# Performance work log

Measured on AMD Instinct MI355X. Metric: run time of the kernel, lower is better.

## Reference

```python
import jax, jax.numpy as jnp
import numpy as np

N = 8192          # points per cloud
IN_C = 256        # in_channels
OUT_C = 256       # out_channels
SC = IN_C // 4    # shortcut_out_channels
KNN = 32          # neighbors gathered per point
KP = 15           # kernel points (standard KPConv)
RADIUS = 0.12
EXTENT = RADIUS * 2.0 / 2.5   # radius * kp_extent / conv_radius
NEG_SLOPE = 0.1
EPS = 1e-5


def setup_inputs() -> dict:
    key = jax.random.key(0)
    ks = jax.random.split(key, 10)
    src = jax.random.normal(ks[0], (N, IN_C), jnp.float32)
    tgt = jax.random.normal(ks[1], (N, IN_C), jnp.float32)
    src_coords = jax.random.uniform(ks[2], (N, 3), jnp.float32)
    tgt_coords = jax.random.uniform(ks[3], (N, 3), jnp.float32)
    W_in = jax.random.normal(ks[4], (IN_C, SC), jnp.float32) / np.sqrt(IN_C)
    b_in = jnp.zeros((SC,), jnp.float32)
    kernel_pts = jax.random.normal(ks[5], (KP, 3), jnp.float32) * (0.7 * EXTENT)
    W_kp = jax.random.normal(ks[6], (KP, SC, SC), jnp.float32) / np.sqrt(KP * SC)
    W_out = jax.random.normal(ks[7], (SC, OUT_C), jnp.float32) / np.sqrt(SC)
    b_out = jnp.zeros((OUT_C,), jnp.float32)
    gamma = jnp.ones((OUT_C,), jnp.float32)
    beta = jnp.zeros((OUT_C,), jnp.float32)
    return dict(src=src, tgt=tgt, src_coords=src_coords, tgt_coords=tgt_coords,
                W_in=W_in, b_in=b_in, kernel_pts=kernel_pts, W_kp=W_kp,
                W_out=W_out, b_out=b_out, gamma=gamma, beta=beta)


def _one_cloud(x, coords, W_in, b_in, kernel_pts, W_kp, W_out, b_out, gamma, beta):
    # 1x1 conv in: [N, IN_C] -> [N, SC]
    h = x @ W_in + b_in

    # neighbor search: kNN by squared distance, masked to the conv radius
    d2 = jnp.sum((coords[:, None, :] - coords[None, :, :]) ** 2, axis=-1)  # [N, N]
    _, idx = jax.lax.top_k(-d2, KNN)                                       # [N, KNN]
    nb_coords = coords[idx]                                                # [N, KNN, 3]
    rel = nb_coords - coords[:, None, :]                                   # [N, KNN, 3]
    in_range = jnp.sum(rel ** 2, axis=-1) <= RADIUS ** 2                   # [N, KNN]

    # KPConv: linear correlation to kernel points, masked neighbor aggregate
    diff = rel[:, :, None, :] - kernel_pts[None, None, :, :]               # [N, KNN, KP, 3]
    dist = jnp.sqrt(jnp.sum(diff ** 2, axis=-1))                           # [N, KNN, KP]
    infl = jnp.maximum(1.0 - dist / EXTENT, 0.0) * in_range[:, :, None]    # [N, KNN, KP]
    nb_feats = h[idx]                                                      # [N, KNN, SC]
    agg = jnp.einsum('nkp,nkc->npc', infl, nb_feats)                       # [N, KP, SC]
    h = jnp.einsum('npc,pcd->nd', agg, W_kp)                               # [N, SC]

    # 1x1 conv out: [N, SC] -> [N, OUT_C]
    y = h @ W_out + b_out

    # batch norm over points (training-mode statistics) + affine
    mu = jnp.mean(y, axis=0)
    var = jnp.mean((y - mu) ** 2, axis=0)
    y = gamma * (y - mu) * jax.lax.rsqrt(var + EPS) + beta

    # leaky relu
    return jnp.where(y > 0, y, NEG_SLOPE * y)


def reference(src, tgt, src_coords, tgt_coords, W_in, b_in, kernel_pts, W_kp,
              W_out, b_out, gamma, beta):
    params = (W_in, b_in, kernel_pts, W_kp, W_out, b_out, gamma, beta)
    s = _one_cloud(src, src_coords, *params)
    t = _one_cloud(tgt, tgt_coords, *params)
    return (s, t, src_coords, tgt_coords)
```

## Files before the change

kernel.cpp:

```cpp
#include <hip/hip_runtime.h>
#include <stdint.h>

#define NPTS 8192
#define KNN 32
#define KPN 15
#define SCC 64
#define OUTC 256
#define R2F 0.0144f
#define INV_EXT (1.0f/0.096f)
#define SCAP 128
#define NT 8
#define COB 32
#define GD 8
#define NCELL (GD*GD*GD)
#define KJ (KPN*SCC)
#define AGP 968

typedef float  f32x4  __attribute__((ext_vector_type(4)));
typedef __bf16 bf16x8 __attribute__((ext_vector_type(8)));

__device__ __forceinline__ int cell_of(float x) {
  int c = (int)(x * (float)GD);
  return c < 0 ? 0 : (c > GD-1 ? GD-1 : c);
}

__global__ __launch_bounds__(256) void prep_k(
    const float* __restrict__ scd, const float* __restrict__ tcd,
    float* __restrict__ out,
    const float* __restrict__ Wkp, __bf16* __restrict__ WkpT,
    const float* __restrict__ Win, __bf16* __restrict__ WinF)
{
  int b = blockIdx.x, t = threadIdx.x;
  if (b < 192) {
    int i = b*256 + t;
    out[i] = (i < NPTS*3) ? scd[i] : tcd[i - NPTS*3];
  } else if (b < 432) {
    int i = (b - 192)*256 + t;
    int j = i >> 6, d = i & 63;
    WkpT[(size_t)d*KJ + j] = (__bf16)Wkp[i];
  } else {
    int i = (b - 432)*256 + t;
    int j = i & 7, lane = (i >> 3) & 63, cc = i >> 9;
    int kc = cc >> 2, ct = cc & 3;
    int g16 = lane >> 4, p = lane & 15;
    int k = kc*32 + g16*8 + j;
    WinF[i] = (__bf16)Win[(size_t)k*64 + ct*16 + p];
  }
}

__global__ __launch_bounds__(1024) void grid_build(
    const float* __restrict__ cA, const float* __restrict__ cB,
    unsigned int* __restrict__ starts,
    unsigned int* __restrict__ cursor,
    float* __restrict__ stats)
{
  __shared__ unsigned int hcnt[2][NCELL];
  __shared__ unsigned int a[NCELL], b[NCELL];
  int t = threadIdx.x;
  if (t < NCELL) { hcnt[0][t] = 0u; hcnt[1][t] = 0u; }
  stats[t] = 0.f;
  __syncthreads();
  for (int i = t; i < 2*NPTS; i += 1024) {
    int cloud = i >> 13, n = i & 8191;
    const float* coords = cloud ? cB : cA;
    int cx = cell_of(coords[(size_t)n*3]);
    int cy = cell_of(coords[(size_t)n*3+1]);
    int cz = cell_of(coords[(size_t)n*3+2]);
    atomicAdd(&hcnt[cloud][(cz*GD + cy)*GD + cx], 1u);
  }
  __syncthreads();
  for (int cloud = 0; cloud < 2; ++cloud) {
    if (t < NCELL) a[t] = hcnt[cloud][t];
    __syncthreads();
    unsigned int *s = a, *d = b;
    for (int off = 1; off < NCELL; off <<= 1) {
      if (t < NCELL) {
        unsigned int x = s[t];
        if (t >= off) x += s[t - off];
        d[t] = x;
      }
      __syncthreads();
      unsigned int* tmp = s; s = d; d = tmp;
    }
    if (t < NCELL) {
      unsigned int inc = s[t];
      unsigned int exc = inc - hcnt[cloud][t];
      starts[cloud*520 + t] = exc;
      cursor[cloud*NCELL + t] = exc;
      if (t == NCELL-1) starts[cloud*520 + NCELL] = inc;
    }
    __syncthreads();
  }
}

__global__ __launch_bounds__(256) void grid_scatter(
    const float* __restrict__ cA, const float* __restrict__ cB,
    unsigned int* __restrict__ cursor, float4* __restrict__ sorted)
{
  int i = blockIdx.x*256 + threadIdx.x;
  int cloud = i >> 13, n = i & 8191;
  const float* coords = cloud ? cB : cA;
  float x = coords[(size_t)n*3], y = coords[(size_t)n*3+1], z = coords[(size_t)n*3+2];
  int cell = (cell_of(z)*GD + cell_of(y))*GD + cell_of(x);
  unsigned int slot = atomicAdd(&cursor[cloud*NCELL + cell], 1u);
  sorted[(size_t)cloud*NPTS + slot] = make_float4(x, y, z, __int_as_float(n));
}

__global__ __launch_bounds__(256) void knn_convin_k(
    const float* __restrict__ cA, const float* __restrict__ cB,
    const unsigned int* __restrict__ starts, const float4* __restrict__ sorted,
    short* __restrict__ fidx,
    const float* __restrict__ src, const float* __restrict__ tgt,
    const __bf16* __restrict__ WinF, const float* __restrict__ bin,
    __bf16* __restrict__ h)
{
  __shared__ unsigned long long surv[4][SCAP];
  int bId = blockIdx.x;
  int t = threadIdx.x, w = t >> 6, lane = t & 63;
  if (bId >= 4096) {
    int rt = (bId - 4096)*4 + w;
    int row0 = rt*16;
    const float* x = (row0 >> 13) ? tgt : src;
    int n0 = row0 & 8191;
    int g16 = lane >> 4, p = lane & 15;
    const float* xrow = x + (size_t)(n0 + p)*256;
    f32x4 acc[4];
    #pragma unroll
    for (int ct = 0; ct < 4; ++ct) {
      float bb = bin[ct*16 + p];
      acc[ct] = (f32x4){bb, bb, bb, bb};
    }
    #pragma unroll
    for (int kc = 0; kc < 8; ++kc) {
      float4 xa = *(const float4*)(xrow + kc*32 + g16*8);
      float4 xb = *(const float4*)(xrow + kc*32 + g16*8 + 4);
      bf16x8 af;
      af[0]=(__bf16)xa.x; af[1]=(__bf16)xa.y; af[2]=(__bf16)xa.z; af[3]=(__bf16)xa.w;
      af[4]=(__bf16)xb.x; af[5]=(__bf16)xb.y; af[6]=(__bf16)xb.z; af[7]=(__bf16)xb.w;
      #pragma unroll
      for (int ct = 0; ct < 4; ++ct) {
        bf16x8 bf = *(const bf16x8*)(WinF + (size_t)(kc*4 + ct)*512 + lane*8);
        acc[ct] = __builtin_amdgcn_mfma_f32_16x16x32_bf16(af, bf, acc[ct], 0,0,0);
      }
    }
    #pragma unroll
    for (int ct = 0; ct < 4; ++ct)
      #pragma unroll
      for (int r = 0; r < 4; ++r)
        h[(size_t)(row0 + g16*4 + r)*SCC + ct*16 + p] = (__bf16)acc[ct][r];
    return;
  }
  int q = bId*4 + w;
  int cloud = q >> 13, n = q & 8191;
  const float* coords = cloud ? cB : cA;
  float qx = coords[(size_t)n*3];
  float qy = coords[(size_t)n*3+1];
  float qz = coords[(size_t)n*3+2];
  int cx = cell_of(qx), cy = cell_of(qy), cz = cell_of(qz);
  const unsigned int* st = starts + cloud*520;
  const float4* sp = sorted + (size_t)cloud*NPTS;
  int c0 = cx > 0 ? cx-1 : 0;
  int c1 = cx < GD-1 ? cx+1 : GD-1;
  unsigned int cnt = 0;
  for (int dz = -1; dz <= 1; ++dz) {
    int zz = cz + dz; if (zz < 0 || zz > GD-1) continue;
    for (int dy = -1; dy <= 1; ++dy) {
      int yy = cy + dy; if (yy < 0 || yy > GD-1) continue;
      int rb = (zz*GD + yy)*GD;
      unsigned int s = st[rb + c0];
      unsigned int e = st[rb + c1 + 1];
      for (unsigned int jj = s; jj < e; jj += 64) {
        unsigned int j = jj + lane;
        bool keep = false; float d2 = 0.f; unsigned int oi = 0;
        if (j < e) {
          float4 p4 = sp[j];
          float dx = qx-p4.x, dyy = qy-p4.y, dzz = qz-p4.z;
          d2 = fmaf(dx, dx, fmaf(dyy, dyy, dzz*dzz));
          oi = __float_as_uint(p4.w);
          keep = (d2 <= R2F);
        }
        unsigned long long m = __ballot(keep);
        if (keep) {
          unsigned int before = __builtin_amdgcn_mbcnt_hi(
              (unsigned int)(m >> 32),
              __builtin_amdgcn_mbcnt_lo((unsigned int)m, 0u));
          unsigned int pos = cnt + before;
          if (pos < SCAP)
            surv[w][pos] = ((unsigned long long)__float_as_uint(d2) << 32) | oi;
        }
        cnt += (unsigned int)__popcll(m);
      }
    }
  }
  int C = (int)cnt; if (C > SCAP) C = SCAP;
  unsigned long long k0 = (lane      < C) ? surv[w][lane]      : ~0ULL;
  unsigned long long k1 = (lane + 64 < C) ? surv[w][lane + 64] : ~0ULL;
  int r0 = 0, r1 = 0;
  for (int j = 0; j < C; ++j) {
    unsigned long long kj = surv[w][j];
    r0 += (kj < k0);
    r1 += (kj < k1);
  }
  size_t g = (size_t)cloud*NPTS + n;
  if (k0 != ~0ULL && r0 < KNN) fidx[g*KNN + r0] = (short)(k0 & 0xffffu);
  if (k1 != ~0ULL && r1 < KNN) fidx[g*KNN + r1] = (short)(k1 & 0xffffu);
  if (lane >= C && lane < KNN) fidx[g*KNN + lane] = (short)-1;
}

__global__ __launch_bounds__(512, 4) void kpconv_fused(
    const float* __restrict__ cA, const float* __restrict__ cB,
    const float* __restrict__ kpts, const short* __restrict__ fidx,
    const __bf16* __restrict__ h, const __bf16* __restrict__ WkpT,
    float* __restrict__ h2)
{
  __shared__ __bf16 agg_s[NT][AGP];
  __shared__ float  red2[2*4*16*17];
  int t = threadIdx.x;
  int w = t >> 6, lane = t & 63;
  int gq = blockIdx.x*NT + w;
  int cloud = gq >> 13, n = gq & 8191;
  const float* coords = cloud ? cB : cA;
  int idxreg = fidx[(size_t)gq*KNN + (lane & 31)];
  float qx = coords[(size_t)n*3];
  float qy = coords[(size_t)n*3+1];
  float qz = coords[(size_t)n*3+2];
  int g16 = lane >> 4;
  int p   = lane & 15;
  int pc  = p < KPN ? p : 0;
  float kpx = kpts[pc*3], kpy = kpts[pc*3+1], kpz = kpts[pc*3+2];
  bf16x8 afrag;
  int idxs[8];
  #pragma unroll
  for (int j = 0; j < 8; ++j) {
    int k = g16*8 + j;
    int idx = __shfl(idxreg, k);
    idxs[j] = idx < 0 ? 0 : idx;
    float wv = 0.f;
    if (idx >= 0 && p < KPN) {
      float rx = coords[(size_t)idx*3]   - qx;
      float ry = coords[(size_t)idx*3+1] - qy;
      float rz = coords[(size_t)idx*3+2] - qz;
      float dx = rx - kpx, dy = ry - kpy, dz = rz - kpz;
      float d = sqrtf(fmaf(dx, dx, fmaf(dy, dy, dz*dz)));
      wv = fmaxf(1.0f - d*INV_EXT, 0.0f);
    }
    afrag[j] = (__bf16)wv;
  }
  bf16x8 bfrag0, bfrag1, bfrag2, bfrag3;
  #pragma unroll
  for (int j = 0; j < 8; ++j) {
    const __bf16* hrow = h + ((size_t)(cloud*NPTS + idxs[j]))*SCC + p;
    bfrag0[j] = hrow[0];
    bfrag1[j] = hrow[16];
    bfrag2[j] = hrow[32];
    bfrag3[j] = hrow[48];
  }
  f32x4 acc0 = {0.f,0.f,0.f,0.f}, acc1 = acc0, acc2 = acc0, acc3 = acc0;
  acc0 = __builtin_amdgcn_mfma_f32_16x16x32_bf16(afrag, bfrag0, acc0, 0, 0, 0);
  acc1 = __builtin_amdgcn_mfma_f32_16x16x32_bf16(afrag, bfrag1, acc1, 0, 0, 0);
  acc2 = __builtin_amdgcn_mfma_f32_16x16x32_bf16(afrag, bfrag2, acc2, 0, 0, 0);
  acc3 = __builtin_amdgcn_mfma_f32_16x16x32_bf16(afrag, bfrag3, acc3, 0, 0, 0);
  #pragma unroll
  for (int r = 0; r < 4; ++r) {
    int pp = g16*4 + r;
    if (pp < KPN) {
      agg_s[w][pp*SCC +      p] = (__bf16)acc0[r];
      agg_s[w][pp*SCC + 16 + p] = (__bf16)acc1[r];
      agg_s[w][pp*SCC + 32 + p] = (__bf16)acc2[r];
      agg_s[w][pp*SCC + 48 + p] = (__bf16)acc3[r];
    }
  }
  int dt = w & 3, kh = w >> 2;
  const __bf16* arow = WkpT + (size_t)(dt*16 + p)*KJ + kh*480 + g16*8;
  bf16x8 afB[15];
  #pragma unroll
  for (int s = 0; s < 15; ++s) afB[s] = *(const bf16x8*)(arow + s*32);
  __syncthreads();
  {
    int ptb = p & 7;
    const __bf16* brow = &agg_s[ptb][kh*480 + g16*8];
    f32x4 accB = {0.f,0.f,0.f,0.f};
    #pragma unroll
    for (int s = 0; s < 15; ++s) {
      bf16x8 bfr = *(const bf16x8*)(brow + s*32);
      accB = __builtin_amdgcn_mfma_f32_16x16x32_bf16(afB[s], bfr, accB, 0, 0, 0);
    }
    if (p < 8) {
      #pragma unroll
      for (int r = 0; r < 4; ++r)
        red2[((kh*4 + dt)*16 + g16*4 + r)*17 + p] = accB[r];
    }
  }
  __syncthreads();
  {
    int pt = t >> 6, d = t & 63;
    float v = red2[d*17 + pt] + red2[(64 + d)*17 + pt];
    h2[((size_t)blockIdx.x*NT + pt)*SCC + d] = v;
  }
}

__global__ __launch_bounds__(512) void conv_out_bn(
    const float* __restrict__ h2, const float* __restrict__ W,
    const float* __restrict__ b, float* __restrict__ y,
    float* __restrict__ stats)
{
  __shared__ float w_s[SCC*OUTC];
  __shared__ float h_s[COB][SCC];
  __shared__ float rs_s[2][OUTC];
  __shared__ float rs2_s[2][OUTC];
  int t = threadIdx.x;
  int d = t & 255, rg = t >> 8;
  int row0 = blockIdx.x*COB;
  int cloud = (int)(blockIdx.x >> 8);
  {
    const float4* gw = (const float4*)W;
    float4* lw = (float4*)w_s;
    #pragma unroll
    for (int i = 0; i < 8; ++i) lw[t + 512*i] = gw[t + 512*i];
    const float4* gh = (const float4*)(h2 + (size_t)row0*SCC);
    ((float4*)h_s)[t] = gh[t];
  }
  __syncthreads();
  float acc[16];
  float bb = b[d];
  #pragma unroll
  for (int r = 0; r < 16; ++r) acc[r] = bb;
  int rb = rg*16;
  #pragma unroll 4
  for (int c4 = 0; c4 < 16; ++c4) {
    float w0 = w_s[(c4*4+0)*OUTC + d];
    float w1 = w_s[(c4*4+1)*OUTC + d];
    float w2 = w_s[(c4*4+2)*OUTC + d];
    float w3 = w_s[(c4*4+3)*OUTC + d];
    #pragma unroll
    for (int r = 0; r < 16; ++r) {
      float4 hv = *(const float4*)&h_s[rb + r][c4*4];
      acc[r] = fmaf(hv.x,w0, fmaf(hv.y,w1, fmaf(hv.z,w2, fmaf(hv.w,w3, acc[r]))));
    }
  }
  float s = 0.f, s2 = 0.f;
  #pragma unroll
  for (int r = 0; r < 16; ++r) {
    float v = acc[r];
    y[((size_t)row0 + rb + r)*OUTC + d] = v;
    s += v; s2 = fmaf(v, v, s2);
  }
  rs_s[rg][d] = s; rs2_s[rg][d] = s2;
  __syncthreads();
  if (rg == 0) {
    atomicAdd(&stats[cloud*512 + d],       s  + rs_s[1][d]);
    atomicAdd(&stats[cloud*512 + 256 + d], s2 + rs2_s[1][d]);
  }
}

__global__ __launch_bounds__(256) void bn_apply_k(
    float* __restrict__ y, const float* __restrict__ stats,
    const float* __restrict__ gamma, const float* __restrict__ beta)
{
  size_t e = (size_t)blockIdx.x*256 + threadIdx.x;
  int c = (int)(e & 255);
  int cloud = (int)(e >> 21);
  float s  = stats[cloud*512 + c];
  float s2 = stats[cloud*512 + 256 + c];
  float mu  = s * (1.0f/NPTS);
  float var = fmaxf(s2 * (1.0f/NPTS) - mu*mu, 0.f);
  float sc = gamma[c] * rsqrtf(var + 1e-5f);
  float sh = beta[c] - mu*sc;
  float v = fmaf(y[e], sc, sh);
  v = v > 0.f ? v : 0.1f*v;
  y[e] = v;
}

extern "C" void kernel_launch(void* const* d_in, const int* in_sizes, int n_in,
                              void* d_out, int out_size, void* d_ws, size_t ws_size,
                              hipStream_t stream)
{
  (void)in_sizes; (void)n_in; (void)out_size; (void)ws_size;
  const float* src   = (const float*)d_in[0];
  const float* tgt   = (const float*)d_in[1];
  const float* scd   = (const float*)d_in[2];
  const float* tcd   = (const float*)d_in[3];
  const float* W_in  = (const float*)d_in[4];
  const float* b_in  = (const float*)d_in[5];
  const float* kpts  = (const float*)d_in[6];
  const float* W_kp  = (const float*)d_in[7];
  const float* W_out = (const float*)d_in[8];
  const float* b_out = (const float*)d_in[9];
  const float* gamma = (const float*)d_in[10];
  const float* beta  = (const float*)d_in[11];

  char* ws = (char*)d_ws;
  __bf16* h    = (__bf16*)ws;
  float* h2    = (float*)(ws + (4u<<20));
  short* fidx  = (short*)(ws + (8u<<20));
  float* stats = (float*)(ws + (9u<<20));
  __bf16* WkpT = (__bf16*)(ws + (9u<<20) + (64u<<10));
  __bf16* WinF = (__bf16*)(ws + (9u<<20) + (256u<<10));
  unsigned int* starts = (unsigned int*)(ws + (4u<<20) + (8u<<10));
  unsigned int* cursor = (unsigned int*)(ws + (4u<<20) + (16u<<10));
  float4* sorted       = (float4*)(ws + (4u<<20) + (32u<<10));

  float* yout = (float*)d_out;

  prep_k<<<496, 256, 0, stream>>>(scd, tcd, yout + (size_t)2*NPTS*OUTC,
                                  W_kp, WkpT, W_in, WinF);
  grid_build<<<1, 1024, 0, stream>>>(scd, tcd, starts, cursor, stats);
  grid_scatter<<<64, 256, 0, stream>>>(scd, tcd, cursor, sorted);
  knn_convin_k<<<4352, 256, 0, stream>>>(scd, tcd, starts, sorted, fidx,
                                         src, tgt, WinF, b_in, h);
  kpconv_fused<<<2048, 512, 0, stream>>>(scd, tcd, kpts, fidx, h, WkpT, h2);
  conv_out_bn<<<512, 512, 0, stream>>>(h2, W_out, b_out, yout, stats);
  bn_apply_k<<<16384, 256, 0, stream>>>(yout, stats, gamma, beta);
}
```

Baseline: 204.0 us.

## Pack coords as float4, vectorize h gather, reorder conv-in blocks first

Writes a padded float4 copy of the coordinates during grid scatter so the kNN and KPConv kernels load each point in one access instead of three scalar loads. The conv-in output h is stored in a permuted channel layout so each neighbor's four channels are fetched with one 8-byte load. The conv-in blocks are moved to the start of the grid, and the WkpT fragment loads now happen inside the MMA loop instead of being preloaded before the barrier, which lowers register pressure but drops the min-blocks launch hint. The cost is an extra coordinate buffer write and possibly exposed weight-load latency after the barrier.

```diff
diff --git a/kernel.cpp b/kernel.cpp
--- a/kernel.cpp
+++ b/kernel.cpp
@@ -18,6 +18,7 @@
 
 typedef float  f32x4  __attribute__((ext_vector_type(4)));
 typedef __bf16 bf16x8 __attribute__((ext_vector_type(8)));
+typedef __bf16 bf16x4 __attribute__((ext_vector_type(4)));
 
 __device__ __forceinline__ int cell_of(float x) {
   int c = (int)(x * (float)GD);
@@ -95,19 +96,21 @@
 
 __global__ __launch_bounds__(256) void grid_scatter(
     const float* __restrict__ cA, const float* __restrict__ cB,
-    unsigned int* __restrict__ cursor, float4* __restrict__ sorted)
+    unsigned int* __restrict__ cursor, float4* __restrict__ sorted,
+    float4* __restrict__ coords4)
 {
   int i = blockIdx.x*256 + threadIdx.x;
   int cloud = i >> 13, n = i & 8191;
   const float* coords = cloud ? cB : cA;
   float x = coords[(size_t)n*3], y = coords[(size_t)n*3+1], z = coords[(size_t)n*3+2];
+  coords4[(size_t)cloud*NPTS + n] = make_float4(x, y, z, 0.f);
   int cell = (cell_of(z)*GD + cell_of(y))*GD + cell_of(x);
   unsigned int slot = atomicAdd(&cursor[cloud*NCELL + cell], 1u);
   sorted[(size_t)cloud*NPTS + slot] = make_float4(x, y, z, __int_as_float(n));
 }
 
 __global__ __launch_bounds__(256) void knn_convin_k(
-    const float* __restrict__ cA, const float* __restrict__ cB,
+    const float4* __restrict__ coords4,
     const unsigned int* __restrict__ starts, const float4* __restrict__ sorted,
     short* __restrict__ fidx,
     const float* __restrict__ src, const float* __restrict__ tgt,
@@ -117,8 +120,8 @@
   __shared__ unsigned long long surv[4][SCAP];
   int bId = blockIdx.x;
   int t = threadIdx.x, w = t >> 6, lane = t & 63;
-  if (bId >= 4096) {
-    int rt = (bId - 4096)*4 + w;
+  if (bId < 256) {
+    int rt = bId*4 + w;
     int row0 = rt*16;
     const float* x = (row0 >> 13) ? tgt : src;
     int n0 = row0 & 8191;
@@ -144,18 +147,18 @@
       }
     }
     #pragma unroll
-    for (int ct = 0; ct < 4; ++ct)
-      #pragma unroll
-      for (int r = 0; r < 4; ++r)
-        h[(size_t)(row0 + g16*4 + r)*SCC + ct*16 + p] = (__bf16)acc[ct][r];
+    for (int r = 0; r < 4; ++r) {
+      bf16x4 o;
+      o[0] = (__bf16)acc[0][r]; o[1] = (__bf16)acc[1][r];
+      o[2] = (__bf16)acc[2][r]; o[3] = (__bf16)acc[3][r];
+      *(bf16x4*)(h + (size_t)(row0 + g16*4 + r)*SCC + p*4) = o;
+    }
     return;
   }
-  int q = bId*4 + w;
+  int q = (bId - 256)*4 + w;
   int cloud = q >> 13, n = q & 8191;
-  const float* coords = cloud ? cB : cA;
-  float qx = coords[(size_t)n*3];
-  float qy = coords[(size_t)n*3+1];
-  float qz = coords[(size_t)n*3+2];
+  float4 qc = coords4[(size_t)cloud*NPTS + n];
+  float qx = qc.x, qy = qc.y, qz = qc.z;
   int cx = cell_of(qx), cy = cell_of(qy), cz = cell_of(qz);
   const unsigned int* st = starts + cloud*520;
   const float4* sp = sorted + (size_t)cloud*NPTS;
@@ -207,8 +210,8 @@
   if (lane >= C && lane < KNN) fidx[g*KNN + lane] = (short)-1;
 }
 
-__global__ __launch_bounds__(512, 4) void kpconv_fused(
-    const float* __restrict__ cA, const float* __restrict__ cB,
+__global__ __launch_bounds__(512) void kpconv_fused(
+    const float4* __restrict__ coords4,
     const float* __restrict__ kpts, const short* __restrict__ fidx,
     const __bf16* __restrict__ h, const __bf16* __restrict__ WkpT,
     float* __restrict__ h2)
@@ -219,11 +222,10 @@
   int w = t >> 6, lane = t & 63;
   int gq = blockIdx.x*NT + w;
   int cloud = gq >> 13, n = gq & 8191;
-  const float* coords = cloud ? cB : cA;
+  const float4* c4 = coords4 + (size_t)cloud*NPTS;
   int idxreg = fidx[(size_t)gq*KNN + (lane & 31)];
-  float qx = coords[(size_t)n*3];
-  float qy = coords[(size_t)n*3+1];
-  float qz = coords[(size_t)n*3+2];
+  float4 qc = c4[n];
+  float qx = qc.x, qy = qc.y, qz = qc.z;
   int g16 = lane >> 4;
   int p   = lane & 15;
   int pc  = p < KPN ? p : 0;
@@ -235,12 +237,12 @@
     int k = g16*8 + j;
     int idx = __shfl(idxreg, k);
     idxs[j] = idx < 0 ? 0 : idx;
+    float4 nc = c4[idxs[j]];
     float wv = 0.f;
     if (idx >= 0 && p < KPN) {
-      float rx = coords[(size_t)idx*3]   - qx;
-      float ry = coords[(size_t)idx*3+1] - qy;
-      float rz = coords[(size_t)idx*3+2] - qz;
-      float dx = rx - kpx, dy = ry - kpy, dz = rz - kpz;
+      float dx = (nc.x - qx) - kpx;
+      float dy = (nc.y - qy) - kpy;
+      float dz = (nc.z - qz) - kpz;
       float d = sqrtf(fmaf(dx, dx, fmaf(dy, dy, dz*dz)));
       wv = fmaxf(1.0f - d*INV_EXT, 0.0f);
     }
@@ -249,11 +251,11 @@
   bf16x8 bfrag0, bfrag1, bfrag2, bfrag3;
   #pragma unroll
   for (int j = 0; j < 8; ++j) {
-    const __bf16* hrow = h + ((size_t)(cloud*NPTS + idxs[j]))*SCC + p;
-    bfrag0[j] = hrow[0];
-    bfrag1[j] = hrow[16];
-    bfrag2[j] = hrow[32];
-    bfrag3[j] = hrow[48];
+    bf16x4 hv = *(const bf16x4*)(h + ((size_t)(cloud*NPTS + idxs[j]))*SCC + p*4);
+    bfrag0[j] = hv[0];
+    bfrag1[j] = hv[1];
+    bfrag2[j] = hv[2];
+    bfrag3[j] = hv[3];
   }
   f32x4 acc0 = {0.f,0.f,0.f,0.f}, acc1 = acc0, acc2 = acc0, acc3 = acc0;
   acc0 = __builtin_amdgcn_mfma_f32_16x16x32_bf16(afrag, bfrag0, acc0, 0, 0, 0);
@@ -270,20 +272,18 @@
       agg_s[w][pp*SCC + 48 + p] = (__bf16)acc3[r];
     }
   }
-  int dt = w & 3, kh = w >> 2;
-  const __bf16* arow = WkpT + (size_t)(dt*16 + p)*KJ + kh*480 + g16*8;
-  bf16x8 afB[15];
-  #pragma unroll
-  for (int s = 0; s < 15; ++s) afB[s] = *(const bf16x8*)(arow + s*32);
   __syncthreads();
   {
+    int dt = w & 3, kh = w >> 2;
     int ptb = p & 7;
+    const __bf16* arow = WkpT + (size_t)(dt*16 + p)*KJ + kh*480 + g16*8;
     const __bf16* brow = &agg_s[ptb][kh*480 + g16*8];
     f32x4 accB = {0.f,0.f,0.f,0.f};
     #pragma unroll
     for (int s = 0; s < 15; ++s) {
+      bf16x8 af = *(const bf16x8*)(arow + s*32);
       bf16x8 bfr = *(const bf16x8*)(brow + s*32);
-      accB = __builtin_amdgcn_mfma_f32_16x16x32_bf16(afB[s], bfr, accB, 0, 0, 0);
+      accB = __builtin_amdgcn_mfma_f32_16x16x32_bf16(af, bfr, accB, 0, 0, 0);
     }
     if (p < 8) {
       #pragma unroll
@@ -396,6 +396,7 @@
   float* stats = (float*)(ws + (9u<<20));
   __bf16* WkpT = (__bf16*)(ws + (9u<<20) + (64u<<10));
   __bf16* WinF = (__bf16*)(ws + (9u<<20) + (256u<<10));
+  float4* coords4 = (float4*)(ws + (9u<<20) + (512u<<10));
   unsigned int* starts = (unsigned int*)(ws + (4u<<20) + (8u<<10));
   unsigned int* cursor = (unsigned int*)(ws + (4u<<20) + (16u<<10));
   float4* sorted       = (float4*)(ws + (4u<<20) + (32u<<10));
@@ -405,10 +406,10 @@
   prep_k<<<496, 256, 0, stream>>>(scd, tcd, yout + (size_t)2*NPTS*OUTC,
                                   W_kp, WkpT, W_in, WinF);
   grid_build<<<1, 1024, 0, stream>>>(scd, tcd, starts, cursor, stats);
-  grid_scatter<<<64, 256, 0, stream>>>(scd, tcd, cursor, sorted);
-  knn_convin_k<<<4352, 256, 0, stream>>>(scd, tcd, starts, sorted, fidx,
+  grid_scatter<<<64, 256, 0, stream>>>(scd, tcd, cursor, sorted, coords4);
+  knn_convin_k<<<4352, 256, 0, stream>>>(coords4, starts, sorted, fidx,
                                          src, tgt, WinF, b_in, h);
-  kpconv_fused<<<2048, 512, 0, stream>>>(scd, tcd, kpts, fidx, h, WkpT, h2);
+  kpconv_fused<<<2048, 512, 0, stream>>>(coords4, kpts, fidx, h, WkpT, h2);
   conv_out_bn<<<512, 512, 0, stream>>>(h2, W_out, b_out, yout, stats);
   bn_apply_k<<<16384, 256, 0, stream>>>(yout, stats, gamma, beta);
 }
```

After: 202.9 us. About the same (-0.5%).
